# Kernel tuning notes

Hardware: AMD Instinct MI355X
Metric: run time of the kernel (lower is better)

The kernel has to match this reference:

```python
import jax, jax.numpy as jnp
import numpy as np

B, CIN, H, W = 4, 128, 256, 256
CH = 96
N = H * W


def _grid_edges(h, w):
    # 4-connected grid, both directions (matches the module's maze_edges lists)
    idx = np.arange(h * w, dtype=np.int32).reshape(h, w)
    l, r = idx[:, :-1].ravel(), idx[:, 1:].ravel()
    u, d = idx[:-1, :].ravel(), idx[1:, :].ravel()
    src = np.concatenate([l, r, u, d])
    dst = np.concatenate([r, l, d, u])
    return np.stack([src, dst])  # [2, E]


def setup_inputs() -> dict:
    key = jax.random.key(0)
    k1, k2, k3 = jax.random.split(key, 3)
    glorot1 = (6.0 / (CIN + CH)) ** 0.5
    glorot2 = (6.0 / (CH + CH)) ** 0.5
    return {
        "x": jax.random.normal(k1, (B, CIN, H, W), dtype=jnp.float32),
        "edge_index": jnp.asarray(_grid_edges(H, W)),
        "W1": jax.random.uniform(k2, (CIN, CH), jnp.float32, -glorot1, glorot1),
        "b1": jnp.zeros((CH,), jnp.float32),
        "W2": jax.random.uniform(k3, (CH, CH), jnp.float32, -glorot2, glorot2),
        "b2": jnp.zeros((CH,), jnp.float32),
    }


def _gcn_conv(h, Wt, b, src, dst, enorm, snorm, n):
    # h: [B, N, Cin] -> PyG GCNConv: D^{-1/2}(A+I)D^{-1/2} (h W) + b
    h = h @ Wt                                   # [B, N, Co]
    msg = h[:, src, :] * enorm[None, :, None]    # gather + edge norm
    agg = jax.vmap(lambda m: jax.ops.segment_sum(m, dst, num_segments=n))(msg)
    return agg + snorm[None, :, None] * h + b    # self-loop term + bias


def reference(x, edge_index, W1, b1, W2, b2):
    b_, c, hgt, wid = x.shape
    n = hgt * wid
    src, dst = edge_index[0], edge_index[1]
    # degrees with self-loops
    deg = jax.ops.segment_sum(jnp.ones_like(src, dtype=x.dtype), dst, num_segments=n) + 1.0
    dinv = jax.lax.rsqrt(deg)
    enorm = dinv[src] * dinv[dst]  # per-edge norm
    snorm = 1.0 / deg              # self-loop norm
    xf = x.reshape(b_, c, n).transpose(0, 2, 1)  # [B, N, C]
    h = jax.nn.relu(_gcn_conv(xf, W1, b1, src, dst, enorm, snorm, n))
    out = _gcn_conv(h, W2, b2, src, dst, enorm, snorm, n)
    return out  # [B, N, CH]
```

## Files before the change

### kernel.cpp

```cpp
#include <hip/hip_runtime.h>
#include <hip/hip_bf16.h>


#define Nn  65536
#define Bb  4

typedef __attribute__((ext_vector_type(8))) short short8;
typedef __attribute__((ext_vector_type(4))) float float4v;

__device__ __forceinline__ float dinv_at(int i, int j) {
    int deg = 1 + (i > 0) + (i < 255) + (j > 0) + (j < 255);
    return rsqrtf((float)deg);
}
__device__ __forceinline__ unsigned short f2bf(float f) {
    __hip_bfloat16 h = __float2bfloat16(f);
    return *reinterpret_cast<unsigned short*>(&h);
}
__device__ __forceinline__ float bf2f(unsigned short u) {
    return __uint_as_float(((unsigned)u) << 16);
}

__global__ void conv_w(const float* __restrict__ W1, const float* __restrict__ W2,
                       unsigned short* __restrict__ wt1, unsigned short* __restrict__ wt2) {
    int t = blockIdx.x * 256 + threadIdx.x;
    if (t < 128 * 96) { int k = t / 96, c = t - k * 96; wt1[c * 128 + k] = f2bf(W1[t]); }
    if (t < 96 * 96)  { int k = t / 96, c = t - k * 96; wt2[c * 96  + k] = f2bf(W2[t]); }
}

template <int K, int NCHUNK, bool FIRST>
__global__ __launch_bounds__(256, 3) void gcn_mfma(
    const void* __restrict__ inp,
    const unsigned short* __restrict__ wtg,
    const float* __restrict__ bias,
    void* __restrict__ outp)
{
    constexpr int SPITCH = 268;
    __shared__ unsigned int sd[2][16 * SPITCH];

    const int t = threadIdx.x, w = t >> 6, l = t & 63;

    const int n_  = blockIdx.x;
    const int xcd = n_ & 7;
    const int p_  = n_ >> 3;
    const int s_  = p_ & 1;
    const int rl  = (p_ >> 1) & 15;
    const int g_  = p_ >> 5;
    const int b   = g_ & 3;
    const int row = (g_ >> 2) * 128 + xcd * 16 + rl;
    const int cout0 = s_ * 48;
    const int n0 = row << 8;

    constexpr int NPL = FIRST ? 4 : 8;
    const int jb = FIRST ? (l * 4) : ((l & 31) * 8);
    float cw[NPL], lw[NPL], rw[NPL], uw[NPL], dw_[NPL];
#pragma unroll
    for (int tn = 0; tn < NPL; ++tn) {
        int j = jb + tn;
        float dc = dinv_at(row, j);
        cw[tn]  = dc * dc;
        lw[tn]  = (j > 0)     ? dc * dinv_at(row, j - 1) : 0.f;
        rw[tn]  = (j < 255)   ? dc * dinv_at(row, j + 1) : 0.f;
        uw[tn]  = (row > 0)   ? dc * dinv_at(row - 1, j) : 0.f;
        dw_[tn] = (row < 255) ? dc * dinv_at(row + 1, j) : 0.f;
    }
    const int rup = (row > 0)   ? -256 : 0;
    const int rdn = (row < 255) ?  256 : 0;

    float4v acc[12];
#pragma unroll
    for (int q_ = 0; q_ < 12; ++q_) acc[q_] = (float4v){0.f, 0.f, 0.f, 0.f};

    const size_t ibase = (size_t)b * K * Nn + n0;
    const int q = l >> 4, m = l & 15;

    for (int ch = 0; ch < NCHUNK; ++ch) {
        unsigned int* sb = sd[ch & 1];

        if (FIRST) {
            const float* xp = (const float*)inp;
#pragma unroll
            for (int p = 0; p < 4; ++p) {
                const int kp = w * 4 + p;
                float y[2][4];
#pragma unroll
                for (int par = 0; par < 2; ++par) {
                    const int k = ch * 32 + kp * 2 + par;
                    const float* pl = xp + ibase + (size_t)k * Nn + 4 * l;
                    const float4 c = *(const float4*)pl;
                    const float4 u = *(const float4*)(pl + rup);
                    const float4 d = *(const float4*)(pl + rdn);
                    const float lm = __shfl_up(c.w, 1);
                    const float rp = __shfl_down(c.x, 1);
                    const float cc[4] = {c.x, c.y, c.z, c.w};
                    const float uu[4] = {u.x, u.y, u.z, u.w};
                    const float dd[4] = {d.x, d.y, d.z, d.w};
                    const float lf[4] = {lm, c.x, c.y, c.z};
                    const float rg[4] = {c.y, c.z, c.w, rp};
#pragma unroll
                    for (int tn = 0; tn < 4; ++tn)
                        y[par][tn] = cw[tn]*cc[tn] + lw[tn]*lf[tn] + rw[tn]*rg[tn]
                                   + uw[tn]*uu[tn] + dw_[tn]*dd[tn];
                }
                unsigned pk[4];
#pragma unroll
                for (int tn = 0; tn < 4; ++tn)
                    pk[tn] = (unsigned)f2bf(y[0][tn]) | ((unsigned)f2bf(y[1][tn]) << 16);
                *(short8*)&sb[kp * SPITCH + 4 * l] = *(short8*)pk;
            }
        } else {
            const unsigned short* hp = (const unsigned short*)inp;
#pragma unroll
            for (int p = 0; p < 4; ++p) {
                const int kp = w * 4 + p;
                const int k = ch * 32 + kp * 2 + (l >> 5);
                const unsigned short* pl = hp + ibase + (size_t)k * Nn + 8 * (l & 31);
                const short8 c8 = *(const short8*)pl;
                const short8 u8 = *(const short8*)(pl + rup);
                const short8 d8 = *(const short8*)(pl + rdn);
                float cc[8], uu[8], dd[8];
#pragma unroll
                for (int tn = 0; tn < 8; ++tn) {
                    cc[tn] = bf2f((unsigned short)c8[tn]);
                    uu[tn] = bf2f((unsigned short)u8[tn]);
                    dd[tn] = bf2f((unsigned short)d8[tn]);
                }
                const float lm = bf2f((unsigned short)__shfl_up((int)(unsigned short)c8[7], 1));
                const float rp = bf2f((unsigned short)__shfl_down((int)(unsigned short)c8[0], 1));
                float y[8];
#pragma unroll
                for (int tn = 0; tn < 8; ++tn) {
                    const float lf = (tn == 0) ? lm : cc[tn - 1];
                    const float rg = (tn == 7) ? rp : cc[tn + 1];
                    y[tn] = cw[tn]*cc[tn] + lw[tn]*lf + rw[tn]*rg
                          + uw[tn]*uu[tn] + dw_[tn]*dd[tn];
                }
                unsigned pk[8];
#pragma unroll
                for (int tn = 0; tn < 8; ++tn) {
                    const float hi = __shfl(y[tn], (l & 31) + 32);
                    pk[tn] = (unsigned)f2bf(y[tn]) | ((unsigned)f2bf(hi) << 16);
                }
                if (l < 32) {
                    *(short8*)&sb[kp * SPITCH + 8 * (l & 31)]     = *(short8*)&pk[0];
                    *(short8*)&sb[kp * SPITCH + 8 * (l & 31) + 4] = *(short8*)&pk[4];
                }
            }
        }

        short8 wf[3];
#pragma unroll
        for (int mt = 0; mt < 3; ++mt)
            wf[mt] = *(const short8*)&wtg[(size_t)(cout0 + mt * 16 + m) * K + ch * 32 + q * 8];

        __syncthreads();

#pragma unroll
        for (int ct = 0; ct < 4; ++ct) {
            const int nodem = (w * 4 + ct) * 16 + m;
            union { unsigned u[4]; short8 s; } df;
#pragma unroll
            for (int jj = 0; jj < 4; ++jj)
                df.u[jj] = sb[(q * 4 + jj) * SPITCH + nodem];
#pragma unroll
            for (int mt = 0; mt < 3; ++mt) {
                if (FIRST)
                    acc[ct * 3 + mt] = __builtin_amdgcn_mfma_f32_16x16x32_bf16(
                        wf[mt], df.s, acc[ct * 3 + mt], 0, 0, 0);
                else
                    acc[ct * 3 + mt] = __builtin_amdgcn_mfma_f32_16x16x32_bf16(
                        df.s, wf[mt], acc[ct * 3 + mt], 0, 0, 0);
            }
        }
    }

    if (FIRST) {
        unsigned short* hb = (unsigned short*)outp + (size_t)b * 96 * Nn + n0;
#pragma unroll
        for (int ct = 0; ct < 4; ++ct) {
            const int node = (w * 4 + ct) * 16 + m;
#pragma unroll
            for (int mt = 0; mt < 3; ++mt)
#pragma unroll
                for (int r = 0; r < 4; ++r) {
                    const int cout = cout0 + mt * 16 + q * 4 + r;
                    const float v = acc[ct * 3 + mt][r] + bias[cout];
                    hb[(size_t)cout * Nn + node] = f2bf(fmaxf(v, 0.f));
                }
        }
    } else {
        float* ob = (float*)outp + ((size_t)b * Nn + n0) * 96;
#pragma unroll
        for (int nt = 0; nt < 4; ++nt)
#pragma unroll
            for (int mt = 0; mt < 3; ++mt) {
                const int cout = cout0 + mt * 16 + m;
                const float bv = bias[cout];
#pragma unroll
                for (int r = 0; r < 4; ++r) {
                    const int node = (w * 4 + nt) * 16 + q * 4 + r;
                    ob[(size_t)node * 96 + cout] = acc[nt * 3 + mt][r] + bv;
                }
            }
    }
}

extern "C" void kernel_launch(void* const* d_in, const int* in_sizes, int n_in,
                              void* d_out, int out_size, void* d_ws, size_t ws_size,
                              hipStream_t stream) {
    const float* x  = (const float*)d_in[0];
    const float* W1 = (const float*)d_in[2];
    const float* b1 = (const float*)d_in[3];
    const float* W2 = (const float*)d_in[4];
    const float* b2 = (const float*)d_in[5];
    float* out = (float*)d_out;

    unsigned short* h   = (unsigned short*)d_ws;
    unsigned short* wt1 = (unsigned short*)((char*)d_ws + 50331648);
    unsigned short* wt2 = (unsigned short*)((char*)d_ws + 50331648 + 24576);

    conv_w<<<48, 256, 0, stream>>>(W1, W2, wt1, wt2);
    gcn_mfma<128, 4, true ><<<2048, 256, 0, stream>>>(x, wt1, b1, h);
    gcn_mfma< 96, 3, false><<<2048, 256, 0, stream>>>(h, wt2, b2, out);
}
```

Baseline: 301.3 us.

## Software-pipeline stencil loads two steps ahead and simplify degree-weight computation

```diff
diff --git a/kernel.cpp b/kernel.cpp
--- a/kernel.cpp
+++ b/kernel.cpp
@@ -35,7 +35,7 @@
     void* __restrict__ outp)
 {
     constexpr int SPITCH = 268;
-    __shared__ unsigned int sd[2][16 * SPITCH];
+    __shared__ unsigned int sdm[2][16 * SPITCH];
 
     const int t = threadIdx.x, w = t >> 6, l = t & 63;
 
@@ -50,19 +50,22 @@
     const int cout0 = s_ * 48;
     const int n0 = row << 8;
 
-    constexpr int NPL = FIRST ? 4 : 8;
-    const int jb = FIRST ? (l * 4) : ((l & 31) * 8);
-    float cw[NPL], lw[NPL], rw[NPL], uw[NPL], dw_[NPL];
-#pragma unroll
-    for (int tn = 0; tn < NPL; ++tn) {
-        int j = jb + tn;
-        float dc = dinv_at(row, j);
-        cw[tn]  = dc * dc;
-        lw[tn]  = (j > 0)     ? dc * dinv_at(row, j - 1) : 0.f;
-        rw[tn]  = (j < 255)   ? dc * dinv_at(row, j + 1) : 0.f;
-        uw[tn]  = (row > 0)   ? dc * dinv_at(row - 1, j) : 0.f;
-        dw_[tn] = (row < 255) ? dc * dinv_at(row + 1, j) : 0.f;
-    }
+    const float dI  = dinv_at(row, 1);
+    const float dE  = dinv_at(row, 0);
+    const float dUi = (row > 0)   ? dinv_at(row - 1, 1) : 0.f;
+    const float dUe = (row > 0)   ? dinv_at(row - 1, 0) : 0.f;
+    const float dDi = (row < 255) ? dinv_at(row + 1, 1) : 0.f;
+    const float dDe = (row < 255) ? dinv_at(row + 1, 0) : 0.f;
+
+    const int  lj = FIRST ? l : (l & 31);
+    const bool eL = (lj == 0), eR = (lj == (FIRST ? 63 : 31));
+    const float dC0 = eL ? dE : dI, dU0 = eL ? dUe : dUi, dD0 = eL ? dDe : dDi;
+    const float dL0 = eL ? 0.f : dI;
+    const float dL1 = eL ? dE  : dI;
+    const float dRm = eR ? dE  : dI;
+    const float dCl = eR ? dE : dI, dUl = eR ? dUe : dUi, dDl = eR ? dDe : dDi;
+    const float dRl = eR ? 0.f : dI;
+
     const int rup = (row > 0)   ? -256 : 0;
     const int rdn = (row < 255) ?  256 : 0;
 
@@ -73,50 +76,104 @@
     const size_t ibase = (size_t)b * K * Nn + n0;
     const int q = l >> 4, m = l & 15;
 
-    for (int ch = 0; ch < NCHUNK; ++ch) {
-        unsigned int* sb = sd[ch & 1];
-
-        if (FIRST) {
-            const float* xp = (const float*)inp;
-#pragma unroll
-            for (int p = 0; p < 4; ++p) {
-                const int kp = w * 4 + p;
-                float y[2][4];
+    constexpr int T = NCHUNK * 4;
+    short8 wf[3];
+
+    if constexpr (FIRST) {
+        const float* xp = (const float*)inp;
+        float4 sc[3][2], su[3][2], sv[3][2];
+
+#define GI1(IT, SL) do {                                                     \
+        const int kp_i = w * 4 + ((IT) & 3);                                 \
+        _Pragma("unroll")                                                    \
+        for (int par = 0; par < 2; ++par) {                                  \
+            const int k_i = ((IT) >> 2) * 32 + kp_i * 2 + par;               \
+            const float* pl_ = xp + ibase + (size_t)k_i * Nn + 4 * l;        \
+            sc[SL][par] = *(const float4*)pl_;                               \
+            su[SL][par] = *(const float4*)(pl_ + rup);                       \
+            sv[SL][par] = *(const float4*)(pl_ + rdn);                       \
+        } } while (0)
+
+        GI1(0, 0); GI1(1, 1);
+#pragma unroll
+        for (int it = 0; it < T; ++it) {
+            if ((it & 3) == 0) {
+                const int ch = it >> 2;
+#pragma unroll
+                for (int mt = 0; mt < 3; ++mt)
+                    wf[mt] = *(const short8*)&wtg[(size_t)(cout0 + mt * 16 + m) * K + ch * 32 + q * 8];
+            }
+            if (it + 2 < T) { GI1(it + 2, (it + 2) % 3); }
+            {
+                const int sl_ = it % 3;
+                const int kp_c = w * 4 + (it & 3);
+                unsigned int* sb = sdm[(it >> 2) & 1];
+                float y2[2][4];
 #pragma unroll
                 for (int par = 0; par < 2; ++par) {
-                    const int k = ch * 32 + kp * 2 + par;
-                    const float* pl = xp + ibase + (size_t)k * Nn + 4 * l;
-                    const float4 c = *(const float4*)pl;
-                    const float4 u = *(const float4*)(pl + rup);
-                    const float4 d = *(const float4*)(pl + rdn);
+                    const float4 c = sc[sl_][par], uu = su[sl_][par], dd = sv[sl_][par];
                     const float lm = __shfl_up(c.w, 1);
                     const float rp = __shfl_down(c.x, 1);
-                    const float cc[4] = {c.x, c.y, c.z, c.w};
-                    const float uu[4] = {u.x, u.y, u.z, u.w};
-                    const float dd[4] = {d.x, d.y, d.z, d.w};
-                    const float lf[4] = {lm, c.x, c.y, c.z};
-                    const float rg[4] = {c.y, c.z, c.w, rp};
-#pragma unroll
-                    for (int tn = 0; tn < 4; ++tn)
-                        y[par][tn] = cw[tn]*cc[tn] + lw[tn]*lf[tn] + rw[tn]*rg[tn]
-                                   + uw[tn]*uu[tn] + dw_[tn]*dd[tn];
+                    y2[par][0] = dC0 * (dC0 * c.x + dL0 * lm  + dI  * c.y + dU0 * uu.x + dD0 * dd.x);
+                    y2[par][1] = dI  * (dI  * c.y + dL1 * c.x + dI  * c.z + dUi * uu.y + dDi * dd.y);
+                    y2[par][2] = dI  * (dI  * c.z + dI  * c.y + dRm * c.w + dUi * uu.z + dDi * dd.z);
+                    y2[par][3] = dCl * (dCl * c.w + dI  * c.z + dRl * rp  + dUl * uu.w + dDl * dd.w);
                 }
                 unsigned pk[4];
 #pragma unroll
                 for (int tn = 0; tn < 4; ++tn)
-                    pk[tn] = (unsigned)f2bf(y[0][tn]) | ((unsigned)f2bf(y[1][tn]) << 16);
-                *(short8*)&sb[kp * SPITCH + 4 * l] = *(short8*)pk;
-            }
-        } else {
-            const unsigned short* hp = (const unsigned short*)inp;
-#pragma unroll
-            for (int p = 0; p < 4; ++p) {
-                const int kp = w * 4 + p;
-                const int k = ch * 32 + kp * 2 + (l >> 5);
-                const unsigned short* pl = hp + ibase + (size_t)k * Nn + 8 * (l & 31);
-                const short8 c8 = *(const short8*)pl;
-                const short8 u8 = *(const short8*)(pl + rup);
-                const short8 d8 = *(const short8*)(pl + rdn);
+                    pk[tn] = (unsigned)f2bf(y2[0][tn]) | ((unsigned)f2bf(y2[1][tn]) << 16);
+                *(short8*)&sb[kp_c * SPITCH + 4 * l] = *(short8*)pk;
+            }
+            if ((it & 3) == 3) {
+                asm volatile("s_waitcnt lgkmcnt(0)" ::: "memory");
+                __builtin_amdgcn_s_barrier();
+                asm volatile("" ::: "memory");
+                __builtin_amdgcn_sched_barrier(0);
+                unsigned int* sb = sdm[(it >> 2) & 1];
+#pragma unroll
+                for (int ct = 0; ct < 4; ++ct) {
+                    const int nodem = (w * 4 + ct) * 16 + m;
+                    union { unsigned u4[4]; short8 s; } df;
+#pragma unroll
+                    for (int jj = 0; jj < 4; ++jj)
+                        df.u4[jj] = sb[(q * 4 + jj) * SPITCH + nodem];
+#pragma unroll
+                    for (int mt = 0; mt < 3; ++mt)
+                        acc[ct * 3 + mt] = __builtin_amdgcn_mfma_f32_16x16x32_bf16(
+                            wf[mt], df.s, acc[ct * 3 + mt], 0, 0, 0);
+                }
+            }
+        }
+#undef GI1
+    } else {
+        const unsigned short* hp = (const unsigned short*)inp;
+        short8 sc[3], su[3], sv[3];
+
+#define GI2(IT, SL) do {                                                     \
+        const int kp_i = w * 4 + ((IT) & 3);                                 \
+        const int k_i = ((IT) >> 2) * 32 + kp_i * 2 + (l >> 5);              \
+        const unsigned short* pl_ = hp + ibase + (size_t)k_i * Nn + 8 * (l & 31); \
+        sc[SL] = *(const short8*)pl_;                                        \
+        su[SL] = *(const short8*)(pl_ + rup);                                \
+        sv[SL] = *(const short8*)(pl_ + rdn);                                \
+    } while (0)
+
+        GI2(0, 0); GI2(1, 1);
+#pragma unroll
+        for (int it = 0; it < T; ++it) {
+            if ((it & 3) == 0) {
+                const int ch = it >> 2;
+#pragma unroll
+                for (int mt = 0; mt < 3; ++mt)
+                    wf[mt] = *(const short8*)&wtg[(size_t)(cout0 + mt * 16 + m) * K + ch * 32 + q * 8];
+            }
+            if (it + 2 < T) { GI2(it + 2, (it + 2) % 3); }
+            {
+                const int sl_ = it % 3;
+                const int kp_c = w * 4 + (it & 3);
+                unsigned int* sb = sdm[(it >> 2) & 1];
+                const short8 c8 = sc[sl_], u8 = su[sl_], d8 = sv[sl_];
                 float cc[8], uu[8], dd[8];
 #pragma unroll
                 for (int tn = 0; tn < 8; ++tn) {
@@ -127,13 +184,13 @@
                 const float lm = bf2f((unsigned short)__shfl_up((int)(unsigned short)c8[7], 1));
                 const float rp = bf2f((unsigned short)__shfl_down((int)(unsigned short)c8[0], 1));
                 float y[8];
-#pragma unroll
-                for (int tn = 0; tn < 8; ++tn) {
-                    const float lf = (tn == 0) ? lm : cc[tn - 1];
-                    const float rg = (tn == 7) ? rp : cc[tn + 1];
-                    y[tn] = cw[tn]*cc[tn] + lw[tn]*lf + rw[tn]*rg
-                          + uw[tn]*uu[tn] + dw_[tn]*dd[tn];
-                }
+                y[0] = dC0 * (dC0 * cc[0] + dL0 * lm    + dI  * cc[1] + dU0 * uu[0] + dD0 * dd[0]);
+                y[1] = dI  * (dI  * cc[1] + dL1 * cc[0] + dI  * cc[2] + dUi * uu[1] + dDi * dd[1]);
+#pragma unroll
+                for (int tn = 2; tn < 6; ++tn)
+                    y[tn] = dI * (dI * (cc[tn - 1] + cc[tn] + cc[tn + 1]) + dUi * uu[tn] + dDi * dd[tn]);
+                y[6] = dI  * (dI  * cc[6] + dI  * cc[5] + dRm * cc[7] + dUi * uu[6] + dDi * dd[6]);
+                y[7] = dCl * (dCl * cc[7] + dI  * cc[6] + dRl * rp    + dUl * uu[7] + dDl * dd[7]);
                 unsigned pk[8];
 #pragma unroll
                 for (int tn = 0; tn < 8; ++tn) {
@@ -141,39 +198,34 @@
                     pk[tn] = (unsigned)f2bf(y[tn]) | ((unsigned)f2bf(hi) << 16);
                 }
                 if (l < 32) {
-                    *(short8*)&sb[kp * SPITCH + 8 * (l & 31)]     = *(short8*)&pk[0];
-                    *(short8*)&sb[kp * SPITCH + 8 * (l & 31) + 4] = *(short8*)&pk[4];
+                    *(short8*)&sb[kp_c * SPITCH + 8 * (l & 31)]     = *(short8*)&pk[0];
+                    *(short8*)&sb[kp_c * SPITCH + 8 * (l & 31) + 4] = *(short8*)&pk[4];
+                }
+            }
+            if ((it & 3) == 3) {
+                asm volatile("s_waitcnt lgkmcnt(0)" ::: "memory");
+                __builtin_amdgcn_s_barrier();
+                asm volatile("" ::: "memory");
+                __builtin_amdgcn_sched_barrier(0);
+                unsigned int* sb = sdm[(it >> 2) & 1];
+#pragma unroll
+                for (int ct = 0; ct < 4; ++ct) {
+                    const int nodem = (w * 4 + ct) * 16 + m;
+                    union { unsigned u4[4]; short8 s; } df;
+#pragma unroll
+                    for (int jj = 0; jj < 4; ++jj)
+                        df.u4[jj] = sb[(q * 4 + jj) * SPITCH + nodem];
+#pragma unroll
+                    for (int mt = 0; mt < 3; ++mt)
+                        acc[ct * 3 + mt] = __builtin_amdgcn_mfma_f32_16x16x32_bf16(
+                            df.s, wf[mt], acc[ct * 3 + mt], 0, 0, 0);
                 }
             }
         }
-
-        short8 wf[3];
-#pragma unroll
-        for (int mt = 0; mt < 3; ++mt)
-            wf[mt] = *(const short8*)&wtg[(size_t)(cout0 + mt * 16 + m) * K + ch * 32 + q * 8];
-
-        __syncthreads();
-
-#pragma unroll
-        for (int ct = 0; ct < 4; ++ct) {
-            const int nodem = (w * 4 + ct) * 16 + m;
-            union { unsigned u[4]; short8 s; } df;
-#pragma unroll
-            for (int jj = 0; jj < 4; ++jj)
-                df.u[jj] = sb[(q * 4 + jj) * SPITCH + nodem];
-#pragma unroll
-            for (int mt = 0; mt < 3; ++mt) {
-                if (FIRST)
-                    acc[ct * 3 + mt] = __builtin_amdgcn_mfma_f32_16x16x32_bf16(
-                        wf[mt], df.s, acc[ct * 3 + mt], 0, 0, 0);
-                else
-                    acc[ct * 3 + mt] = __builtin_amdgcn_mfma_f32_16x16x32_bf16(
-                        df.s, wf[mt], acc[ct * 3 + mt], 0, 0, 0);
-            }
-        }
+#undef GI2
     }
 
-    if (FIRST) {
+    if constexpr (FIRST) {
         unsigned short* hb = (unsigned short*)outp + (size_t)b * 96 * Nn + n0;
 #pragma unroll
         for (int ct = 0; ct < 4; ++ct) {
```

Result: slower. 357.4 us (+18.6%).

## Merge two output-channel halves into one 512-thread block sharing aggregated tile

Applied to the files above, without the earlier changes.

```diff
diff --git a/kernel.cpp b/kernel.cpp
--- a/kernel.cpp
+++ b/kernel.cpp
@@ -28,41 +28,44 @@
 }
 
 template <int K, int NCHUNK, bool FIRST>
-__global__ __launch_bounds__(256, 3) void gcn_mfma(
+__global__ __launch_bounds__(512, 4) void gcn_mfma(
     const void* __restrict__ inp,
     const unsigned short* __restrict__ wtg,
     const float* __restrict__ bias,
     void* __restrict__ outp)
 {
     constexpr int SPITCH = 268;
-    __shared__ unsigned int sd[2][16 * SPITCH];
+    __shared__ unsigned int sdm[2][16 * SPITCH];
 
     const int t = threadIdx.x, w = t >> 6, l = t & 63;
+    const int wm = w & 3;
+    const int cout0 = (w >> 2) * 48;
 
     const int n_  = blockIdx.x;
     const int xcd = n_ & 7;
     const int p_  = n_ >> 3;
-    const int s_  = p_ & 1;
-    const int rl  = (p_ >> 1) & 15;
-    const int g_  = p_ >> 5;
+    const int rl  = p_ & 15;
+    const int g_  = p_ >> 4;
     const int b   = g_ & 3;
     const int row = (g_ >> 2) * 128 + xcd * 16 + rl;
-    const int cout0 = s_ * 48;
     const int n0 = row << 8;
 
-    constexpr int NPL = FIRST ? 4 : 8;
-    const int jb = FIRST ? (l * 4) : ((l & 31) * 8);
-    float cw[NPL], lw[NPL], rw[NPL], uw[NPL], dw_[NPL];
-#pragma unroll
-    for (int tn = 0; tn < NPL; ++tn) {
-        int j = jb + tn;
-        float dc = dinv_at(row, j);
-        cw[tn]  = dc * dc;
-        lw[tn]  = (j > 0)     ? dc * dinv_at(row, j - 1) : 0.f;
-        rw[tn]  = (j < 255)   ? dc * dinv_at(row, j + 1) : 0.f;
-        uw[tn]  = (row > 0)   ? dc * dinv_at(row - 1, j) : 0.f;
-        dw_[tn] = (row < 255) ? dc * dinv_at(row + 1, j) : 0.f;
-    }
+    const float dI  = dinv_at(row, 1);
+    const float dE  = dinv_at(row, 0);
+    const float dUi = (row > 0)   ? dinv_at(row - 1, 1) : 0.f;
+    const float dUe = (row > 0)   ? dinv_at(row - 1, 0) : 0.f;
+    const float dDi = (row < 255) ? dinv_at(row + 1, 1) : 0.f;
+    const float dDe = (row < 255) ? dinv_at(row + 1, 0) : 0.f;
+
+    const int  lj = FIRST ? l : (l & 31);
+    const bool eL = (lj == 0), eR = (lj == (FIRST ? 63 : 31));
+    const float dC0 = eL ? dE : dI, dU0 = eL ? dUe : dUi, dD0 = eL ? dDe : dDi;
+    const float dL0 = eL ? 0.f : dI;
+    const float dL1 = eL ? dE  : dI;
+    const float dRm = eR ? dE  : dI;
+    const float dCl = eR ? dE : dI, dUl = eR ? dUe : dUi, dDl = eR ? dDe : dDi;
+    const float dRl = eR ? 0.f : dI;
+
     const int rup = (row > 0)   ? -256 : 0;
     const int rdn = (row < 255) ?  256 : 0;
 
@@ -73,14 +76,20 @@
     const size_t ibase = (size_t)b * K * Nn + n0;
     const int q = l >> 4, m = l & 15;
 
+    short8 wf[3];
+
     for (int ch = 0; ch < NCHUNK; ++ch) {
-        unsigned int* sb = sd[ch & 1];
+        unsigned int* sb = sdm[ch & 1];
+
+#pragma unroll
+        for (int mt = 0; mt < 3; ++mt)
+            wf[mt] = *(const short8*)&wtg[(size_t)(cout0 + mt * 16 + m) * K + ch * 32 + q * 8];
 
         if (FIRST) {
             const float* xp = (const float*)inp;
 #pragma unroll
-            for (int p = 0; p < 4; ++p) {
-                const int kp = w * 4 + p;
+            for (int p = 0; p < 2; ++p) {
+                const int kp = w * 2 + p;
                 float y[2][4];
 #pragma unroll
                 for (int par = 0; par < 2; ++par) {
@@ -91,15 +100,10 @@
                     const float4 d = *(const float4*)(pl + rdn);
                     const float lm = __shfl_up(c.w, 1);
                     const float rp = __shfl_down(c.x, 1);
-                    const float cc[4] = {c.x, c.y, c.z, c.w};
-                    const float uu[4] = {u.x, u.y, u.z, u.w};
-                    const float dd[4] = {d.x, d.y, d.z, d.w};
-                    const float lf[4] = {lm, c.x, c.y, c.z};
-                    const float rg[4] = {c.y, c.z, c.w, rp};
-#pragma unroll
-                    for (int tn = 0; tn < 4; ++tn)
-                        y[par][tn] = cw[tn]*cc[tn] + lw[tn]*lf[tn] + rw[tn]*rg[tn]
-                                   + uw[tn]*uu[tn] + dw_[tn]*dd[tn];
+                    y[par][0] = dC0 * (dC0 * c.x + dL0 * lm  + dI  * c.y + dU0 * u.x + dD0 * d.x);
+                    y[par][1] = dI  * (dI  * c.y + dL1 * c.x + dI  * c.z + dUi * u.y + dDi * d.y);
+                    y[par][2] = dI  * (dI  * c.z + dI  * c.y + dRm * c.w + dUi * u.z + dDi * d.z);
+                    y[par][3] = dCl * (dCl * c.w + dI  * c.z + dRl * rp  + dUl * u.w + dDl * d.w);
                 }
                 unsigned pk[4];
 #pragma unroll
@@ -110,8 +114,8 @@
         } else {
             const unsigned short* hp = (const unsigned short*)inp;
 #pragma unroll
-            for (int p = 0; p < 4; ++p) {
-                const int kp = w * 4 + p;
+            for (int p = 0; p < 2; ++p) {
+                const int kp = w * 2 + p;
                 const int k = ch * 32 + kp * 2 + (l >> 5);
                 const unsigned short* pl = hp + ibase + (size_t)k * Nn + 8 * (l & 31);
                 const short8 c8 = *(const short8*)pl;
@@ -127,13 +131,13 @@
                 const float lm = bf2f((unsigned short)__shfl_up((int)(unsigned short)c8[7], 1));
                 const float rp = bf2f((unsigned short)__shfl_down((int)(unsigned short)c8[0], 1));
                 float y[8];
-#pragma unroll
-                for (int tn = 0; tn < 8; ++tn) {
-                    const float lf = (tn == 0) ? lm : cc[tn - 1];
-                    const float rg = (tn == 7) ? rp : cc[tn + 1];
-                    y[tn] = cw[tn]*cc[tn] + lw[tn]*lf + rw[tn]*rg
-                          + uw[tn]*uu[tn] + dw_[tn]*dd[tn];
-                }
+                y[0] = dC0 * (dC0 * cc[0] + dL0 * lm    + dI  * cc[1] + dU0 * uu[0] + dD0 * dd[0]);
+                y[1] = dI  * (dI  * cc[1] + dL1 * cc[0] + dI  * cc[2] + dUi * uu[1] + dDi * dd[1]);
+#pragma unroll
+                for (int tn = 2; tn < 6; ++tn)
+                    y[tn] = dI * (dI * (cc[tn - 1] + cc[tn] + cc[tn + 1]) + dUi * uu[tn] + dDi * dd[tn]);
+                y[6] = dI  * (dI  * cc[6] + dI  * cc[5] + dRm * cc[7] + dUi * uu[6] + dDi * dd[6]);
+                y[7] = dCl * (dCl * cc[7] + dI  * cc[6] + dRl * rp    + dUl * uu[7] + dDl * dd[7]);
                 unsigned pk[8];
 #pragma unroll
                 for (int tn = 0; tn < 8; ++tn) {
@@ -147,20 +151,18 @@
             }
         }
 
-        short8 wf[3];
-#pragma unroll
-        for (int mt = 0; mt < 3; ++mt)
-            wf[mt] = *(const short8*)&wtg[(size_t)(cout0 + mt * 16 + m) * K + ch * 32 + q * 8];
-
-        __syncthreads();
+        asm volatile("s_waitcnt lgkmcnt(0)" ::: "memory");
+        __builtin_amdgcn_s_barrier();
+        asm volatile("" ::: "memory");
+        __builtin_amdgcn_sched_barrier(0);
 
 #pragma unroll
         for (int ct = 0; ct < 4; ++ct) {
-            const int nodem = (w * 4 + ct) * 16 + m;
-            union { unsigned u[4]; short8 s; } df;
+            const int nodem = (wm * 4 + ct) * 16 + m;
+            union { unsigned u4[4]; short8 s; } df;
 #pragma unroll
             for (int jj = 0; jj < 4; ++jj)
-                df.u[jj] = sb[(q * 4 + jj) * SPITCH + nodem];
+                df.u4[jj] = sb[(q * 4 + jj) * SPITCH + nodem];
 #pragma unroll
             for (int mt = 0; mt < 3; ++mt) {
                 if (FIRST)
@@ -177,7 +179,7 @@
         unsigned short* hb = (unsigned short*)outp + (size_t)b * 96 * Nn + n0;
 #pragma unroll
         for (int ct = 0; ct < 4; ++ct) {
-            const int node = (w * 4 + ct) * 16 + m;
+            const int node = (wm * 4 + ct) * 16 + m;
 #pragma unroll
             for (int mt = 0; mt < 3; ++mt)
 #pragma unroll
@@ -197,7 +199,7 @@
                 const float bv = bias[cout];
 #pragma unroll
                 for (int r = 0; r < 4; ++r) {
-                    const int node = (w * 4 + nt) * 16 + q * 4 + r;
+                    const int node = (wm * 4 + nt) * 16 + q * 4 + r;
                     ob[(size_t)node * 96 + cout] = acc[nt * 3 + mt][r] + bv;
                 }
             }
@@ -219,6 +221,6 @@
     unsigned short* wt2 = (unsigned short*)((char*)d_ws + 50331648 + 24576);
 
     conv_w<<<48, 256, 0, stream>>>(W1, W2, wt1, wt2);
-    gcn_mfma<128, 4, true ><<<2048, 256, 0, stream>>>(x, wt1, b1, h);
-    gcn_mfma< 96, 3, false><<<2048, 256, 0, stream>>>(h, wt2, b2, out);
-}
+    gcn_mfma<128, 4, true ><<<1024, 512, 0, stream>>>(x, wt1, b1, h);
+    gcn_mfma< 96, 3, false><<<1024, 512, 0, stream>>>(h, wt2, b2, out);
+}
```

Result: faster. 276.4 us (-8.3%).
